# Kernel tuning notes

Measured on AMD Instinct MI355X. Metric: run time of the kernel, lower is better.

Reference implementation:

```python
import jax, jax.numpy as jnp
import numpy as np

B, C, H, W = 256, 768, 14, 14
S = 196  # sample_size
HID = 512
OUT = 2


def setup_inputs() -> dict:
    key = jax.random.key(0)
    ks = jax.random.split(key, 10)
    x = jax.random.normal(ks[0], (B, C, H, W), dtype=jnp.float32)
    pxs = jax.random.randint(ks[1], (B, S, 2), 0, H, dtype=jnp.int32)
    pys = jax.random.randint(ks[2], (B, S, 2), 0, H, dtype=jnp.int32)
    scale = 0.02
    W1 = jax.random.normal(ks[3], (2 * C, HID), dtype=jnp.float32) * scale
    b1 = jnp.zeros((HID,), dtype=jnp.float32)
    W2 = jax.random.normal(ks[4], (HID, HID), dtype=jnp.float32) * scale
    b2 = jnp.zeros((HID,), dtype=jnp.float32)
    W3 = jax.random.normal(ks[5], (HID, OUT), dtype=jnp.float32) * scale
    b3 = jnp.zeros((OUT,), dtype=jnp.float32)
    return {"x": x, "W1": W1, "b1": b1, "W2": W2, "b2": b2,
            "W3": W3, "b3": b3, "pxs": pxs, "pys": pys}


def _gather_pts(x_flat, pxy):
    # x_flat: [B, C, H*W]; pxy: [B, S, 2] -> [B, S, C]
    idx = pxy[:, :, 0] * W + pxy[:, :, 1]            # [B, S]
    g = jnp.take_along_axis(x_flat, idx[:, None, :].astype(jnp.int32), axis=2)  # [B, C, S]
    return g.transpose(0, 2, 1)                       # [B, S, C]


def reference(x, W1, b1, W2, b2, W3, b3, pxs, pys):
    x_flat = x.reshape(B, C, H * W)
    ptsx = _gather_pts(x_flat, pxs)                   # [B, S, C]
    ptsy = _gather_pts(x_flat, pys)                   # [B, S, C]
    feats = jnp.concatenate([ptsx, ptsy], axis=2)     # [B, S, 2C]
    h = jax.nn.relu(feats @ W1 + b1)
    h = jax.nn.relu(h @ W2 + b2)
    pred = h @ W3 + b3                                # [B, S, 2]
    predxy = pred.reshape(-1, OUT)                    # [B*S, 2]
    # use_abs=False, normalize=False: deltaxy = (pxs - pys) + (H - 1)
    deltaxy = (pxs - pys).astype(jnp.float32).reshape(-1, 2) + (H - 1)
    return predxy, deltaxy
```

## Files before the change

### kernel.cpp

```cpp
#include <hip/hip_runtime.h>
#include <hip/hip_bf16.h>

typedef __attribute__((ext_vector_type(4))) float f32x4;
typedef __attribute__((ext_vector_type(4))) int   int4v;
typedef __attribute__((ext_vector_type(8))) int   int8v;

__device__ __forceinline__ unsigned char f2fp8(float f) {
    unsigned char s = (__float_as_uint(f) >> 24) & 0x80;
    float a = fabsf(f);
    if (a >= 448.f) return s | 0x7E;
    if (a < 0.015625f) {
        int q = (int)(a * 512.0f + 0.5f);
        return s | (unsigned char)q;
    }
    unsigned int u = __float_as_uint(a);
    u += 0x0007FFFF + ((u >> 20) & 1);
    int e8 = (int)((u >> 23) & 0xFF) - 120;
    if (e8 >= 16) return s | 0x7E;
    return s | (unsigned char)((e8 << 3) | ((u >> 20) & 7));
}
__device__ __forceinline__ void gload_lds16(const void* g, void* l) {
    __builtin_amdgcn_global_load_lds((const __attribute__((address_space(1))) void*)g,
                                     (__attribute__((address_space(3))) void*)l, 16, 0, 0);
}

#define BATCH 256
#define CHAN  768
#define HW    196
#define SPS   196
#define HID   512
#define MROWS 50176
#define K1    1536
#define WSCL  64.0f
#define WINV  0.015625f
#define SC1   0x7F7F7F7F

__global__ void transpose_cast_fp8(const float* __restrict__ in, unsigned char* __restrict__ out,
                                   int K, int N) {
    int idx = blockIdx.x * 256 + threadIdx.x;
    if (idx >= K * N) return;
    int n = idx / K, k = idx - n * K;
    out[idx] = f2fp8(in[(size_t)k * N + n] * WSCL);
}

__global__ __launch_bounds__(256) void gather_feats(const float* __restrict__ x,
                                                    const int* __restrict__ pxs,
                                                    const int* __restrict__ pys,
                                                    const float* __restrict__ b3,
                                                    unsigned char* __restrict__ feats,
                                                    float* __restrict__ out) {
    __shared__ float lds[64 * 197];
    int chunk = blockIdx.x;
    int b     = blockIdx.y;
    int c0 = chunk * 64;
    const float* xb = x + ((size_t)b * CHAN + c0) * HW;
    for (int t = threadIdx.x; t < 64 * HW; t += 256) {
        int j = t / HW, p = t - j * HW;
        lds[j * 197 + p] = xb[t];
    }
    if (chunk == 0) {
        float b30 = b3[0], b31 = b3[1];
        for (int i = threadIdx.x; i < SPS * 2; i += 256) {
            int idx = b * SPS * 2 + i;
            out[idx] = (i & 1) ? b31 : b30;
            out[MROWS * 2 + idx] = (float)(pxs[idx] - pys[idx]) + 13.0f;
        }
    }
    __syncthreads();
    int wid = threadIdx.x >> 6, lane = threadIdx.x & 63;
    int g = lane >> 4;
    int cq = (lane & 15) * 4;
    for (int sb = wid * 4; sb < SPS; sb += 16) {
        int s = sb + g;
        int base = (b * SPS + s) * 2;
        int ix = pxs[base] * 14 + pxs[base + 1];
        int iy = pys[base] * 14 + pys[base + 1];
        const float* lx = lds + cq * 197;
        unsigned int ux = 0, uy = 0;
        ux = __builtin_amdgcn_cvt_pk_fp8_f32(lx[ix],       lx[197 + ix], ux, false);
        ux = __builtin_amdgcn_cvt_pk_fp8_f32(lx[394 + ix], lx[591 + ix], ux, true);
        uy = __builtin_amdgcn_cvt_pk_fp8_f32(lx[iy],       lx[197 + iy], uy, false);
        uy = __builtin_amdgcn_cvt_pk_fp8_f32(lx[394 + iy], lx[591 + iy], uy, true);
        size_t ro = (size_t)(b * SPS + s) * K1;
        *(unsigned int*)(feats + ro + c0 + cq)        = ux;
        *(unsigned int*)(feats + ro + CHAN + c0 + cq) = uy;
    }
}

__global__ __launch_bounds__(256, 2) void gemm_mx(const unsigned char* __restrict__ A,
                                                  const unsigned char* __restrict__ Bt,
                                                  const float* __restrict__ bias,
                                                  unsigned char* __restrict__ C,
                                                  const float* __restrict__ W3,
                                                  float* __restrict__ out,
                                                  int Kd, int predMode) {
    extern __shared__ char smem[];
    const int t = threadIdx.x;
    const int wid = t >> 6, lane = t & 63;
    const int wr = wid >> 1, wc = wid & 1;
    const int lr = lane & 15, lk = lane >> 4;
    const int mBase = (blockIdx.x >> 2) * 128;
    const int nBase = (blockIdx.x & 3) * 128;
    const int nK = Kd >> 7;
    f32x4 acc[4][4] = {};

    auto stage = [&](int buf, int td) {
        char* Ab = smem + buf * 32768;
        char* Bb = Ab + 16384;
        int k0 = td << 7;
        #pragma unroll
        for (int i = 0; i < 4; ++i) {
            int lin = i * 256 + t;
            int row = lin >> 3;
            int cs  = (lin & 7) ^ (row & 7);
            gload_lds16((const char*)A + ((size_t)(mBase + row) * Kd + k0 + cs * 16),
                        Ab + lin * 16);
        }
        #pragma unroll
        for (int i = 0; i < 4; ++i) {
            int lin = i * 256 + t;
            int row = lin >> 3;
            int cs  = (lin & 7) ^ (row & 7);
            gload_lds16((const char*)Bt + ((size_t)(nBase + row) * Kd + k0 + cs * 16),
                        Bb + lin * 16);
        }
    };
    auto compute = [&](int buf) {
        const char* Ab = smem + buf * 32768;
        const char* Bb = Ab + 16384;
        int8v af[4], bfr[4];
        #pragma unroll
        for (int m = 0; m < 4; ++m) {
            int r = wr * 64 + m * 16 + lr;
            const char* p = Ab + r * 128;
            union { int4v h[2]; int8v v; } u;
            u.h[0] = *(const int4v*)(p + (((2 * lk + 0) ^ (r & 7)) * 16));
            u.h[1] = *(const int4v*)(p + (((2 * lk + 1) ^ (r & 7)) * 16));
            af[m] = u.v;
        }
        #pragma unroll
        for (int n = 0; n < 4; ++n) {
            int r = wc * 64 + n * 16 + lr;
            const char* p = Bb + r * 128;
            union { int4v h[2]; int8v v; } u;
            u.h[0] = *(const int4v*)(p + (((2 * lk + 0) ^ (r & 7)) * 16));
            u.h[1] = *(const int4v*)(p + (((2 * lk + 1) ^ (r & 7)) * 16));
            bfr[n] = u.v;
        }
        #pragma unroll
        for (int m = 0; m < 4; ++m)
            #pragma unroll
            for (int n = 0; n < 4; ++n)
                acc[m][n] = __builtin_amdgcn_mfma_scale_f32_16x16x128_f8f6f4(
                    af[m], bfr[n], acc[m][n], 0, 0, 0, SC1, 0, SC1);
    };

    stage(0, 0);
    __syncthreads();
    int cur = 0;
    for (int td = 0; td < nK; ++td) {
        if (td + 1 < nK) stage(cur ^ 1, td + 1);
        compute(cur);
        __syncthreads();
        cur ^= 1;
    }

    if (!predMode) {
        #pragma unroll
        for (int n = 0; n < 4; ++n) {
            int c = nBase + wc * 64 + n * 16 + lr;
            float bv = bias[c];
            #pragma unroll
            for (int m = 0; m < 4; ++m) {
                int r0 = mBase + wr * 64 + m * 16 + lk * 4;
                #pragma unroll
                for (int j = 0; j < 4; ++j)
                    C[(size_t)(r0 + j) * HID + c] = f2fp8(fmaxf(acc[m][n][j] * WINV + bv, 0.f));
            }
        }
    } else {
        float* red = (float*)smem;
        float w3v[4][2], bv[4];
        #pragma unroll
        for (int n = 0; n < 4; ++n) {
            int c = nBase + wc * 64 + n * 16 + lr;
            w3v[n][0] = W3[c * 2 + 0];
            w3v[n][1] = W3[c * 2 + 1];
            bv[n] = bias[c];
        }
        #pragma unroll
        for (int m = 0; m < 4; ++m) {
            #pragma unroll
            for (int j = 0; j < 4; ++j) {
                float p0 = 0.f, p1 = 0.f;
                #pragma unroll
                for (int n = 0; n < 4; ++n) {
                    float v = fmaxf(acc[m][n][j] * WINV + bv[n], 0.f);
                    p0 += v * w3v[n][0];
                    p1 += v * w3v[n][1];
                }
                #pragma unroll
                for (int msk = 1; msk < 16; msk <<= 1) {
                    p0 += __shfl_xor(p0, msk);
                    p1 += __shfl_xor(p1, msk);
                }
                if (lr == 0) {
                    int rl = wr * 64 + m * 16 + lk * 4 + j;
                    red[rl * 4 + wc * 2 + 0] = p0;
                    red[rl * 4 + wc * 2 + 1] = p1;
                }
            }
        }
        __syncthreads();
        if (t < 256) {
            int rl = t >> 1, comp = t & 1;
            float v = red[rl * 4 + 0 * 2 + comp] + red[rl * 4 + 1 * 2 + comp];
            atomicAdd(&out[(size_t)(mBase + rl) * 2 + comp], v);
        }
    }
}

extern "C" void kernel_launch(void* const* d_in, const int* in_sizes, int n_in,
                              void* d_out, int out_size, void* d_ws, size_t ws_size,
                              hipStream_t stream) {
    const float* x  = (const float*)d_in[0];
    const float* W1 = (const float*)d_in[1];
    const float* b1 = (const float*)d_in[2];
    const float* W2 = (const float*)d_in[3];
    const float* b2 = (const float*)d_in[4];
    const float* W3 = (const float*)d_in[5];
    const float* b3 = (const float*)d_in[6];
    const int*  pxs = (const int*)d_in[7];
    const int*  pys = (const int*)d_in[8];
    float* out = (float*)d_out;
    char* ws = (char*)d_ws;

    unsigned char* W1t   = (unsigned char*)(ws + 0);
    unsigned char* W2t   = (unsigned char*)(ws + 786432);
    unsigned char* h1    = (unsigned char*)(ws + 1048576);
    unsigned char* feats = (unsigned char*)(ws + 26738688);

    hipFuncSetAttribute((const void*)gemm_mx,
                        hipFuncAttributeMaxDynamicSharedMemorySize, 65536);

    transpose_cast_fp8<<<(K1 * HID + 255) / 256, 256, 0, stream>>>(W1, W1t, K1, HID);
    transpose_cast_fp8<<<(HID * HID + 255) / 256, 256, 0, stream>>>(W2, W2t, HID, HID);
    gather_feats<<<dim3(12, BATCH), 256, 0, stream>>>(x, pxs, pys, b3, feats, out);
    gemm_mx<<<(MROWS / 128) * 4, 256, 65536, stream>>>(
        feats, W1t, b1, h1, nullptr, nullptr, K1, 0);
    gemm_mx<<<(MROWS / 128) * 4, 256, 65536, stream>>>(
        h1, W2t, b2, nullptr, W3, out, HID, 1);
}
```

Measured before the change: 180.2 us.

## Retile FP8 MX GEMM to 64x256 blocks with 8 waves and packed epilogue

The GEMM block tile changes from 128x128 with 4 waves to 64x256 with 8 waves. Each wave owns a 64x32 output slice, and all waves share the A fragments loaded from LDS. The epilogue replaces the software fp8 conversion with the hardware packed cvt_pk_fp8 instruction. The aim is to change the load balance and the B-tile reuse and to make the ReLU/quantize stage cheaper. In exchange, each block uses more LDS (80KB), which may limit occupancy, and each wave now runs only 8 MFMAs per k-step, which may expose LDS latency.

New measurement: 164.8 us. -8.5%, faster.

```diff
diff --git a/kernel.cpp b/kernel.cpp
--- a/kernel.cpp
+++ b/kernel.cpp
@@ -34,6 +34,7 @@
 #define WSCL  64.0f
 #define WINV  0.015625f
 #define SC1   0x7F7F7F7F
+
 
 __global__ void transpose_cast_fp8(const float* __restrict__ in, unsigned char* __restrict__ out,
                                    int K, int N) {
@@ -87,79 +88,69 @@
     }
 }
 
-__global__ __launch_bounds__(256, 2) void gemm_mx(const unsigned char* __restrict__ A,
-                                                  const unsigned char* __restrict__ Bt,
-                                                  const float* __restrict__ bias,
-                                                  unsigned char* __restrict__ C,
-                                                  const float* __restrict__ W3,
-                                                  float* __restrict__ out,
-                                                  int Kd, int predMode) {
+__global__ __launch_bounds__(512, 2)
+void gemm64(const unsigned char* __restrict__ A,
+            const unsigned char* __restrict__ Bt,
+            const float* __restrict__ bias,
+            unsigned char* __restrict__ C,
+            const float* __restrict__ W3,
+            float* __restrict__ out,
+            int Kd, int predMode) {
     extern __shared__ char smem[];
     const int t = threadIdx.x;
     const int wid = t >> 6, lane = t & 63;
-    const int wr = wid >> 1, wc = wid & 1;
     const int lr = lane & 15, lk = lane >> 4;
-    const int mBase = (blockIdx.x >> 2) * 128;
-    const int nBase = (blockIdx.x & 3) * 128;
+    const int mBase = (blockIdx.x >> 1) * 64;
+    const int nBase = (blockIdx.x & 1) * 256;
     const int nK = Kd >> 7;
-    f32x4 acc[4][4] = {};
-
-    auto stage = [&](int buf, int td) {
-        char* Ab = smem + buf * 32768;
-        char* Bb = Ab + 16384;
-        int k0 = td << 7;
+    f32x4 acc[4][2] = {};
+
+    auto stage = [&](int buf, int kt) {
+        char* Ab = smem + buf * 8192;
+        char* Bb = smem + 16384 + buf * 32768;
+        {
+            int row = t >> 3, cs = (t & 7) ^ (row & 7);
+            gload_lds16(A + (size_t)(mBase + row) * Kd + kt * 128 + cs * 16,
+                        Ab + t * 16);
+        }
         #pragma unroll
         for (int i = 0; i < 4; ++i) {
-            int lin = i * 256 + t;
-            int row = lin >> 3;
-            int cs  = (lin & 7) ^ (row & 7);
-            gload_lds16((const char*)A + ((size_t)(mBase + row) * Kd + k0 + cs * 16),
-                        Ab + lin * 16);
-        }
-        #pragma unroll
-        for (int i = 0; i < 4; ++i) {
-            int lin = i * 256 + t;
-            int row = lin >> 3;
-            int cs  = (lin & 7) ^ (row & 7);
-            gload_lds16((const char*)Bt + ((size_t)(nBase + row) * Kd + k0 + cs * 16),
+            int lin = i * 512 + t, row = lin >> 3, cs = (lin & 7) ^ (row & 7);
+            gload_lds16(Bt + (size_t)(nBase + row) * Kd + kt * 128 + cs * 16,
                         Bb + lin * 16);
         }
+    };
+    auto frag128 = [&](const char* rowp, int r) -> int8v {
+        union { int4v h[2]; int8v v; } u;
+        u.h[0] = *(const int4v*)(rowp + (((2 * lk + 0) ^ (r & 7)) * 16));
+        u.h[1] = *(const int4v*)(rowp + (((2 * lk + 1) ^ (r & 7)) * 16));
+        return u.v;
     };
     auto compute = [&](int buf) {
-        const char* Ab = smem + buf * 32768;
-        const char* Bb = Ab + 16384;
-        int8v af[4], bfr[4];
+        const char* Ab = smem + buf * 8192;
+        const char* Bb = smem + 16384 + buf * 32768;
+        int8v af[4];
         #pragma unroll
         for (int m = 0; m < 4; ++m) {
-            int r = wr * 64 + m * 16 + lr;
-            const char* p = Ab + r * 128;
-            union { int4v h[2]; int8v v; } u;
-            u.h[0] = *(const int4v*)(p + (((2 * lk + 0) ^ (r & 7)) * 16));
-            u.h[1] = *(const int4v*)(p + (((2 * lk + 1) ^ (r & 7)) * 16));
-            af[m] = u.v;
-        }
-        #pragma unroll
-        for (int n = 0; n < 4; ++n) {
-            int r = wc * 64 + n * 16 + lr;
-            const char* p = Bb + r * 128;
-            union { int4v h[2]; int8v v; } u;
-            u.h[0] = *(const int4v*)(p + (((2 * lk + 0) ^ (r & 7)) * 16));
-            u.h[1] = *(const int4v*)(p + (((2 * lk + 1) ^ (r & 7)) * 16));
-            bfr[n] = u.v;
-        }
-        #pragma unroll
-        for (int m = 0; m < 4; ++m)
-            #pragma unroll
-            for (int n = 0; n < 4; ++n)
+            int r = m * 16 + lr;
+            af[m] = frag128(Ab + r * 128, r);
+        }
+        #pragma unroll
+        for (int n = 0; n < 2; ++n) {
+            int r = wid * 32 + n * 16 + lr;
+            int8v bf = frag128(Bb + r * 128, r);
+            #pragma unroll
+            for (int m = 0; m < 4; ++m)
                 acc[m][n] = __builtin_amdgcn_mfma_scale_f32_16x16x128_f8f6f4(
-                    af[m], bfr[n], acc[m][n], 0, 0, 0, SC1, 0, SC1);
+                    af[m], bf, acc[m][n], 0, 0, 0, SC1, 0, SC1);
+        }
     };
 
     stage(0, 0);
     __syncthreads();
     int cur = 0;
-    for (int td = 0; td < nK; ++td) {
-        if (td + 1 < nK) stage(cur ^ 1, td + 1);
+    for (int kt = 0; kt < nK; ++kt) {
+        if (kt + 1 < nK) stage(cur ^ 1, kt + 1);
         compute(cur);
         __syncthreads();
         cur ^= 1;
@@ -167,37 +158,44 @@
 
     if (!predMode) {
         #pragma unroll
-        for (int n = 0; n < 4; ++n) {
-            int c = nBase + wc * 64 + n * 16 + lr;
+        for (int n = 0; n < 2; ++n) {
+            int c = nBase + wid * 32 + n * 16 + lr;
             float bv = bias[c];
             #pragma unroll
             for (int m = 0; m < 4; ++m) {
-                int r0 = mBase + wr * 64 + m * 16 + lk * 4;
+                int r0 = mBase + m * 16 + lk * 4;
+                float v0 = fmaxf(acc[m][n][0] * WINV + bv, 0.f);
+                float v1 = fmaxf(acc[m][n][1] * WINV + bv, 0.f);
+                float v2 = fmaxf(acc[m][n][2] * WINV + bv, 0.f);
+                float v3 = fmaxf(acc[m][n][3] * WINV + bv, 0.f);
+                unsigned int u = __builtin_amdgcn_cvt_pk_fp8_f32(v0, v1, 0u, false);
+                u = __builtin_amdgcn_cvt_pk_fp8_f32(v2, v3, u, true);
                 #pragma unroll
                 for (int j = 0; j < 4; ++j)
-                    C[(size_t)(r0 + j) * HID + c] = f2fp8(fmaxf(acc[m][n][j] * WINV + bv, 0.f));
+                    C[(size_t)(r0 + j) * HID + c] = (unsigned char)((u >> (8 * j)) & 0xff);
             }
         }
     } else {
         float* red = (float*)smem;
-        float w3v[4][2], bv[4];
-        #pragma unroll
-        for (int n = 0; n < 4; ++n) {
-            int c = nBase + wc * 64 + n * 16 + lr;
-            w3v[n][0] = W3[c * 2 + 0];
-            w3v[n][1] = W3[c * 2 + 1];
-            bv[n] = bias[c];
-        }
+        float bv2[2], w30[2], w31[2];
+        #pragma unroll
+        for (int n = 0; n < 2; ++n) {
+            int c = nBase + wid * 32 + n * 16 + lr;
+            bv2[n] = bias[c];
+            w30[n] = W3[c * 2];
+            w31[n] = W3[c * 2 + 1];
+        }
+        __syncthreads();
         #pragma unroll
         for (int m = 0; m < 4; ++m) {
             #pragma unroll
             for (int j = 0; j < 4; ++j) {
                 float p0 = 0.f, p1 = 0.f;
                 #pragma unroll
-                for (int n = 0; n < 4; ++n) {
-                    float v = fmaxf(acc[m][n][j] * WINV + bv[n], 0.f);
-                    p0 += v * w3v[n][0];
-                    p1 += v * w3v[n][1];
+                for (int n = 0; n < 2; ++n) {
+                    float v = fmaxf(acc[m][n][j] * WINV + bv2[n], 0.f);
+                    p0 += v * w30[n];
+                    p1 += v * w31[n];
                 }
                 #pragma unroll
                 for (int msk = 1; msk < 16; msk <<= 1) {
@@ -205,16 +203,19 @@
                     p1 += __shfl_xor(p1, msk);
                 }
                 if (lr == 0) {
-                    int rl = wr * 64 + m * 16 + lk * 4 + j;
-                    red[rl * 4 + wc * 2 + 0] = p0;
-                    red[rl * 4 + wc * 2 + 1] = p1;
+                    int rl = m * 16 + lk * 4 + j;
+                    red[rl * 17 + wid * 2 + 0] = p0;
+                    red[rl * 17 + wid * 2 + 1] = p1;
                 }
             }
         }
         __syncthreads();
-        if (t < 256) {
+        if (t < 128) {
             int rl = t >> 1, comp = t & 1;
-            float v = red[rl * 4 + 0 * 2 + comp] + red[rl * 4 + 1 * 2 + comp];
+            float v = 0.f;
+            #pragma unroll
+            for (int w = 0; w < 8; ++w)
+                v += red[rl * 17 + w * 2 + comp];
             atomicAdd(&out[(size_t)(mBase + rl) * 2 + comp], v);
         }
     }
@@ -240,14 +241,14 @@
     unsigned char* h1    = (unsigned char*)(ws + 1048576);
     unsigned char* feats = (unsigned char*)(ws + 26738688);
 
-    hipFuncSetAttribute((const void*)gemm_mx,
-                        hipFuncAttributeMaxDynamicSharedMemorySize, 65536);
+    hipFuncSetAttribute((const void*)gemm64,
+                        hipFuncAttributeMaxDynamicSharedMemorySize, 81920);
 
     transpose_cast_fp8<<<(K1 * HID + 255) / 256, 256, 0, stream>>>(W1, W1t, K1, HID);
     transpose_cast_fp8<<<(HID * HID + 255) / 256, 256, 0, stream>>>(W2, W2t, HID, HID);
     gather_feats<<<dim3(12, BATCH), 256, 0, stream>>>(x, pxs, pys, b3, feats, out);
-    gemm_mx<<<(MROWS / 128) * 4, 256, 65536, stream>>>(
+    gemm64<<<(MROWS / 64) * 2, 512, 81920, stream>>>(
         feats, W1t, b1, h1, nullptr, nullptr, K1, 0);
-    gemm_mx<<<(MROWS / 128) * 4, 256, 65536, stream>>>(
+    gemm64<<<(MROWS / 64) * 2, 512, 81920, stream>>>(
         h1, W2t, b2, nullptr, W3, out, HID, 1);
 }
```
